# Kernel optimization log

Measured on AMD Instinct MI355X. Metric: run time of the kernel, lower is better.

## Reference

```python
import jax, jax.numpy as jnp
import numpy as np

B, T = 64, 2048
RNN_DIM, EMB_DIM, ATTN_DIM = 1024, 512, 128
N_FILT, KSIZE = 32, 31
PAD = (KSIZE - 1) // 2


def setup_inputs() -> dict:
    key = jax.random.key(0)
    ks = jax.random.split(key, 8)
    s = 0.02
    return {
        "attention_hidden_state": jax.random.normal(ks[0], (B, RNN_DIM), jnp.float32),
        "memory": jax.random.normal(ks[1], (B, T, EMB_DIM), jnp.float32),
        "processed_memory": jax.random.normal(ks[2], (B, T, ATTN_DIM), jnp.float32),
        "attention_weights_cat": jax.random.uniform(ks[3], (B, 2, T), jnp.float32),
        "mask": jnp.zeros((B, T), dtype=bool),
        "Wq": jax.random.normal(ks[4], (ATTN_DIM, RNN_DIM), jnp.float32) * s,
        "Wconv": jax.random.normal(ks[5], (N_FILT, 2, KSIZE), jnp.float32) * s,
        "Wloc": jax.random.normal(ks[6], (ATTN_DIM, N_FILT), jnp.float32) * s,
        "Wv": jax.random.normal(ks[7], (1, ATTN_DIM), jnp.float32) * s,
    }


def reference(attention_hidden_state, memory, processed_memory,
              attention_weights_cat, mask, Wq, Wconv, Wloc, Wv):
    # query projection: [B, rnn] -> [B, 1, attn]
    pq = jnp.einsum("br,ar->ba", attention_hidden_state, Wq)[:, None, :]
    # location conv: [B, 2, T] -> [B, F, T]
    conv = jax.lax.conv_general_dilated(
        attention_weights_cat, Wconv, window_strides=(1,),
        padding=[(PAD, PAD)], dimension_numbers=("NCH", "OIH", "NCH"))
    # [B, T, F] @ Wloc.T -> [B, T, attn]
    ploc = jnp.einsum("bft,af->bta", conv, Wloc)
    # energies: [B, T]
    energies = jnp.einsum("bta,oa->bto", jnp.tanh(pq + ploc + processed_memory), Wv)[..., 0]
    alignment = jnp.where(mask, -jnp.inf, energies)
    attention_weights = jax.nn.softmax(alignment, axis=1)
    # context: [B, emb]
    attention_context = jnp.einsum("bt,bte->be", attention_weights, memory)
    return attention_context, attention_weights
```

## Files before the change

### kernel.cpp

```cpp
#include <hip/hip_runtime.h>
#include <math.h>

#define BB 64
#define TT 2048
#define RNN 1024
#define EMB 512
#define ATTN 128
#define NF 32
#define KS 31
#define PADW 15

#define CHUNK 64
#define NCH (TT / CHUNK)

__device__ __forceinline__ float fast_tanh(float x) {
    float ax = fabsf(x);
    float e = __expf(-2.f * ax);
    float r = (1.f - e) * __builtin_amdgcn_rcpf(1.f + e);
    return copysignf(r, x);
}

__global__ __launch_bounds__(256) void pq_kernel(const float* __restrict__ h,
                                                 const float* __restrict__ Wq,
                                                 float* __restrict__ pq) {
    int b = blockIdx.x >> 2;
    int q = blockIdx.x & 3;
    __shared__ float s_h[RNN];
    for (int i = threadIdx.x; i < RNN; i += 256) s_h[i] = h[b * RNN + i];
    __syncthreads();

    int wave = threadIdx.x >> 6;
    int lane = threadIdx.x & 63;
#pragma unroll 2
    for (int j = 0; j < 8; ++j) {
        int a = q * 32 + wave * 8 + j;
        const float4* wq4 = (const float4*)(Wq + (size_t)a * RNN);
        float acc = 0.f;
#pragma unroll
        for (int i = 0; i < 4; ++i) {
            float4 w4 = wq4[lane + 64 * i];
            float4 h4 = *(const float4*)(s_h + 4 * (lane + 64 * i));
            acc += w4.x * h4.x + w4.y * h4.y + w4.z * h4.z + w4.w * h4.w;
        }
#pragma unroll
        for (int off = 32; off > 0; off >>= 1) acc += __shfl_xor(acc, off, 64);
        if (lane == 0) pq[b * ATTN + a] = acc;
    }
}

__global__ __launch_bounds__(256) void fused_kernel(
    const float* __restrict__ pm,
    const float* __restrict__ awc,
    const float* __restrict__ mem,
    const unsigned char* __restrict__ mask,
    const float* __restrict__ pq,
    const float* __restrict__ Wconv,
    const float* __restrict__ Wloc,
    const float* __restrict__ Wv,
    float* __restrict__ wp,
    float* __restrict__ ms,
    float* __restrict__ cp)
{
    int b = blockIdx.x >> 5;
    int ch = blockIdx.x & 31;
    int t0 = ch * CHUNK;
    int tid = threadIdx.x;

    __shared__ float s_awc[2][CHUNK + 2 * PADW];
    __shared__ float s_conv[CHUNK][36];
    __shared__ float s_e[CHUNK];
    __shared__ float s_p[CHUNK];

    for (int i = tid; i < 2 * (CHUNK + 2 * PADW); i += 256) {
        int c = i / (CHUNK + 2 * PADW);
        int j = i % (CHUNK + 2 * PADW);
        int tg = t0 - PADW + j;
        s_awc[c][j] = (tg >= 0 && tg < TT) ? awc[((size_t)b * 2 + c) * TT + tg] : 0.f;
    }
    __syncthreads();

    {
        int t = tid & 63;
        int fh = tid >> 6;
        float aw[2][KS];
#pragma unroll
        for (int c = 0; c < 2; ++c)
#pragma unroll
            for (int k = 0; k < KS; ++k) aw[c][k] = s_awc[c][t + k];
#pragma unroll
        for (int ff = 0; ff < 8; ++ff) {
            int f = fh * 8 + ff;
            float acc = 0.f;
#pragma unroll
            for (int c = 0; c < 2; ++c)
#pragma unroll
                for (int k = 0; k < KS; ++k)
                    acc += aw[c][k] * Wconv[(f * 2 + c) * KS + k];
            s_conv[t][f] = acc;
        }
    }
    __syncthreads();

    int wave = tid >> 6;
    int lane = tid & 63;

    float wl0[NF], wl1[NF];
#pragma unroll
    for (int f = 0; f < NF; ++f) {
        wl0[f] = Wloc[lane * NF + f];
        wl1[f] = Wloc[(lane + 64) * NF + f];
    }
    float pq0 = pq[b * ATTN + lane], pq1 = pq[b * ATTN + lane + 64];
    float wv0 = Wv[lane], wv1 = Wv[lane + 64];

    float eout = 0.f;
#pragma unroll 2
    for (int i = 0; i < 16; ++i) {
        int tl = wave * 16 + i;
        int tg = t0 + tl;
        float v0 = pq0, v1 = pq1;
        const float4* cv4 = (const float4*)&s_conv[tl][0];
#pragma unroll
        for (int f4 = 0; f4 < 8; ++f4) {
            float4 cv = cv4[f4];
            v0 += cv.x * wl0[f4 * 4 + 0] + cv.y * wl0[f4 * 4 + 1] +
                  cv.z * wl0[f4 * 4 + 2] + cv.w * wl0[f4 * 4 + 3];
            v1 += cv.x * wl1[f4 * 4 + 0] + cv.y * wl1[f4 * 4 + 1] +
                  cv.z * wl1[f4 * 4 + 2] + cv.w * wl1[f4 * 4 + 3];
        }
        const float* pmrow = pm + ((size_t)(b * TT + tg)) * ATTN;
        v0 += pmrow[lane];
        v1 += pmrow[lane + 64];
        float e = wv0 * fast_tanh(v0) + wv1 * fast_tanh(v1);
#pragma unroll
        for (int off = 32; off > 0; off >>= 1) e += __shfl_xor(e, off, 64);
        if (lane == i) eout = e;
    }
    if (lane < 16) {
        int tl = wave * 16 + lane;
        float e = eout;
        if (mask[(size_t)b * TT + t0 + tl] != 0) e = -1e30f;
        s_e[tl] = e;
    }
    __syncthreads();

    float m = s_e[lane];
#pragma unroll
    for (int off = 32; off > 0; off >>= 1) m = fmaxf(m, __shfl_xor(m, off, 64));

    if (tid < CHUNK) {
        float p = __expf(s_e[tid] - m);
        s_p[tid] = p;
        wp[(size_t)b * TT + t0 + tid] = p;
    }
    __syncthreads();

    float ssum = s_p[lane];
#pragma unroll
    for (int off = 32; off > 0; off >>= 1) ssum += __shfl_xor(ssum, off, 64);
    if (tid == 0) {
        ms[(b * NCH + ch) * 2 + 0] = m;
        ms[(b * NCH + ch) * 2 + 1] = ssum;
    }

    int e4 = tid & 127;
    int half = tid >> 7;
    float4 acc = {0.f, 0.f, 0.f, 0.f};
    const float4* m4 = (const float4*)(mem + ((size_t)b * TT + t0) * EMB) +
                       (size_t)half * (EMB / 4) + e4;
#pragma unroll 8
    for (int i = 0; i < CHUNK / 2; ++i) {
        float pv = s_p[2 * i + half];
        float4 mv = m4[(size_t)i * (2 * EMB / 4)];
        acc.x += pv * mv.x;
        acc.y += pv * mv.y;
        acc.z += pv * mv.z;
        acc.w += pv * mv.w;
    }
    float4* cp4 = (float4*)(cp + ((size_t)((ch * 2 + half) * BB + b)) * EMB) + e4;
    *cp4 = acc;
}

__global__ __launch_bounds__(256) void combine_kernel(
    const float* __restrict__ wp, const float* __restrict__ ms,
    const float* __restrict__ cp, float* __restrict__ ctx,
    float* __restrict__ wts) {
    int b = blockIdx.x;
    int tid = threadIdx.x;
    __shared__ float s_m[NCH], s_s[NCH], s_scale[NCH];
    if (tid < NCH) {
        s_m[tid] = ms[(b * NCH + tid) * 2 + 0];
        s_s[tid] = ms[(b * NCH + tid) * 2 + 1];
    }
    __syncthreads();
    float M = -1e30f;
#pragma unroll
    for (int c = 0; c < NCH; ++c) M = fmaxf(M, s_m[c]);
    float S = 0.f;
#pragma unroll
    for (int c = 0; c < NCH; ++c) S += s_s[c] * __expf(s_m[c] - M);
    float invS = 1.f / S;
    if (tid < NCH) s_scale[tid] = __expf(s_m[tid] - M) * invS;
    __syncthreads();

    if (tid < 128) {
        float4 acc = {0.f, 0.f, 0.f, 0.f};
#pragma unroll 8
        for (int c = 0; c < 2 * NCH; ++c) {
            float sc = s_scale[c >> 1];
            float4 v = *((const float4*)(cp + ((size_t)(c * BB + b)) * EMB) + tid);
            acc.x += sc * v.x;
            acc.y += sc * v.y;
            acc.z += sc * v.z;
            acc.w += sc * v.w;
        }
        *((float4*)(ctx + (size_t)b * EMB) + tid) = acc;
    }
#pragma unroll
    for (int i = 0; i < 8; ++i) {
        int t = i * 256 + tid;
        wts[(size_t)b * TT + t] = wp[(size_t)b * TT + t] * s_scale[t >> 6];
    }
}

extern "C" void kernel_launch(void* const* d_in, const int* in_sizes, int n_in,
                              void* d_out, int out_size, void* d_ws, size_t ws_size,
                              hipStream_t stream) {
    const float* h    = (const float*)d_in[0];
    const float* mem  = (const float*)d_in[1];
    const float* pmem = (const float*)d_in[2];
    const float* awc  = (const float*)d_in[3];
    const unsigned char* mask = (const unsigned char*)d_in[4];
    const float* Wq   = (const float*)d_in[5];
    const float* Wcv  = (const float*)d_in[6];
    const float* Wloc = (const float*)d_in[7];
    const float* Wv   = (const float*)d_in[8];

    float* out = (float*)d_out;
    float* ctx = out;
    float* wts = out + BB * EMB;

    float* ws = (float*)d_ws;
    float* pq = ws;
    float* wp = pq + BB * ATTN;
    float* ms = wp + BB * TT;
    float* cp = ms + BB * NCH * 2;

    pq_kernel<<<BB * 4, 256, 0, stream>>>(h, Wq, pq);
    fused_kernel<<<BB * NCH, 256, 0, stream>>>(pmem, awc, mem, mask, pq, Wcv,
                                               Wloc, Wv, wp, ms, cp);
    combine_kernel<<<BB, 256, 0, stream>>>(wp, ms, cp, ctx, wts);
}
```

Before: 126.4 us.

## Make each wave own a 16-step softmax chunk to remove block barriers

Each wave now handles its own 16-timestep chunk end to end: it batches the processed_memory loads, keeps the 16 energies in registers, runs a batched shuffle reduction, computes the local max/sum, and accumulates its own memory context. Three block barriers and the shared-memory energy and probability staging go away, and memory loads per wave become independent. The cost is four times as many partial chunks (128 per batch), so the combine kernel reads more partial context data. The extra registers for the per-wave arrays may pressure the 4-blocks-per-CU launch bound.

```diff
diff --git a/kernel.cpp b/kernel.cpp
--- a/kernel.cpp
+++ b/kernel.cpp
@@ -10,8 +10,9 @@
 #define KS 31
 #define PADW 15
 
-#define CHUNK 64
-#define NCH (TT / CHUNK)
+#define CHW 16
+#define NCH (TT / CHW)
+#define BLK_T 64
 
 __device__ __forceinline__ float fast_tanh(float x) {
     float ax = fabsf(x);
@@ -48,7 +49,7 @@
     }
 }
 
-__global__ __launch_bounds__(256) void fused_kernel(
+__global__ __launch_bounds__(256, 4) void fused_kernel(
     const float* __restrict__ pm,
     const float* __restrict__ awc,
     const float* __restrict__ mem,
@@ -62,26 +63,27 @@
     float* __restrict__ cp)
 {
     int b = blockIdx.x >> 5;
-    int ch = blockIdx.x & 31;
-    int t0 = ch * CHUNK;
+    int chg = blockIdx.x & 31;
+    int t0b = chg * BLK_T;
     int tid = threadIdx.x;
-
-    __shared__ float s_awc[2][CHUNK + 2 * PADW];
-    __shared__ float s_conv[CHUNK][36];
-    __shared__ float s_e[CHUNK];
-    __shared__ float s_p[CHUNK];
-
-    for (int i = tid; i < 2 * (CHUNK + 2 * PADW); i += 256) {
-        int c = i / (CHUNK + 2 * PADW);
-        int j = i % (CHUNK + 2 * PADW);
-        int tg = t0 - PADW + j;
+    int w = tid >> 6;
+    int lane = tid & 63;
+    int ch = chg * 4 + w;
+    int t0w = ch * CHW;
+
+    __shared__ float s_awc[2][BLK_T + 2 * PADW + 2];
+    __shared__ float s_conv[BLK_T][36];
+
+    for (int i = tid; i < 2 * (BLK_T + 2 * PADW); i += 256) {
+        int c = i / (BLK_T + 2 * PADW);
+        int j = i % (BLK_T + 2 * PADW);
+        int tg = t0b - PADW + j;
         s_awc[c][j] = (tg >= 0 && tg < TT) ? awc[((size_t)b * 2 + c) * TT + tg] : 0.f;
     }
     __syncthreads();
 
     {
         int t = tid & 63;
-        int fh = tid >> 6;
         float aw[2][KS];
 #pragma unroll
         for (int c = 0; c < 2; ++c)
@@ -89,7 +91,7 @@
             for (int k = 0; k < KS; ++k) aw[c][k] = s_awc[c][t + k];
 #pragma unroll
         for (int ff = 0; ff < 8; ++ff) {
-            int f = fh * 8 + ff;
+            int f = w * 8 + ff;
             float acc = 0.f;
 #pragma unroll
             for (int c = 0; c < 2; ++c)
@@ -101,9 +103,6 @@
     }
     __syncthreads();
 
-    int wave = tid >> 6;
-    int lane = tid & 63;
-
     float wl0[NF], wl1[NF];
 #pragma unroll
     for (int f = 0; f < NF; ++f) {
@@ -113,72 +112,83 @@
     float pq0 = pq[b * ATTN + lane], pq1 = pq[b * ATTN + lane + 64];
     float wv0 = Wv[lane], wv1 = Wv[lane + 64];
 
-    float eout = 0.f;
-#pragma unroll 2
-    for (int i = 0; i < 16; ++i) {
-        int tl = wave * 16 + i;
-        int tg = t0 + tl;
-        float v0 = pq0, v1 = pq1;
-        const float4* cv4 = (const float4*)&s_conv[tl][0];
-#pragma unroll
-        for (int f4 = 0; f4 < 8; ++f4) {
-            float4 cv = cv4[f4];
-            v0 += cv.x * wl0[f4 * 4 + 0] + cv.y * wl0[f4 * 4 + 1] +
-                  cv.z * wl0[f4 * 4 + 2] + cv.w * wl0[f4 * 4 + 3];
-            v1 += cv.x * wl1[f4 * 4 + 0] + cv.y * wl1[f4 * 4 + 1] +
-                  cv.z * wl1[f4 * 4 + 2] + cv.w * wl1[f4 * 4 + 3];
-        }
-        const float* pmrow = pm + ((size_t)(b * TT + tg)) * ATTN;
-        v0 += pmrow[lane];
-        v1 += pmrow[lane + 64];
-        float e = wv0 * fast_tanh(v0) + wv1 * fast_tanh(v1);
-#pragma unroll
-        for (int off = 32; off > 0; off >>= 1) e += __shfl_xor(e, off, 64);
-        if (lane == i) eout = e;
-    }
-    if (lane < 16) {
-        int tl = wave * 16 + lane;
-        float e = eout;
-        if (mask[(size_t)b * TT + t0 + tl] != 0) e = -1e30f;
-        s_e[tl] = e;
-    }
-    __syncthreads();
-
-    float m = s_e[lane];
-#pragma unroll
-    for (int off = 32; off > 0; off >>= 1) m = fmaxf(m, __shfl_xor(m, off, 64));
-
-    if (tid < CHUNK) {
-        float p = __expf(s_e[tid] - m);
-        s_p[tid] = p;
-        wp[(size_t)b * TT + t0 + tid] = p;
-    }
-    __syncthreads();
-
-    float ssum = s_p[lane];
-#pragma unroll
-    for (int off = 32; off > 0; off >>= 1) ssum += __shfl_xor(ssum, off, 64);
-    if (tid == 0) {
-        ms[(b * NCH + ch) * 2 + 0] = m;
-        ms[(b * NCH + ch) * 2 + 1] = ssum;
-    }
-
-    int e4 = tid & 127;
-    int half = tid >> 7;
-    float4 acc = {0.f, 0.f, 0.f, 0.f};
-    const float4* m4 = (const float4*)(mem + ((size_t)b * TT + t0) * EMB) +
-                       (size_t)half * (EMB / 4) + e4;
-#pragma unroll 8
-    for (int i = 0; i < CHUNK / 2; ++i) {
-        float pv = s_p[2 * i + half];
-        float4 mv = m4[(size_t)i * (2 * EMB / 4)];
-        acc.x += pv * mv.x;
-        acc.y += pv * mv.y;
-        acc.z += pv * mv.z;
-        acc.w += pv * mv.w;
-    }
-    float4* cp4 = (float4*)(cp + ((size_t)((ch * 2 + half) * BB + b)) * EMB) + e4;
-    *cp4 = acc;
+    float e[CHW];
+#pragma unroll
+    for (int h = 0; h < 2; ++h) {
+        float pA[8], pB[8];
+#pragma unroll
+        for (int i = 0; i < 8; ++i) {
+            const float* r = pm + ((size_t)b * TT + t0w + h * 8 + i) * ATTN;
+            pA[i] = r[lane];
+            pB[i] = r[lane + 64];
+        }
+#pragma unroll
+        for (int i = 0; i < 8; ++i) {
+            int tl = w * CHW + h * 8 + i;
+            float v0 = pq0 + pA[i], v1 = pq1 + pB[i];
+            const float4* cv4 = (const float4*)&s_conv[tl][0];
+#pragma unroll
+            for (int f4 = 0; f4 < 8; ++f4) {
+                float4 cv = cv4[f4];
+                v0 += cv.x * wl0[f4 * 4 + 0] + cv.y * wl0[f4 * 4 + 1] +
+                      cv.z * wl0[f4 * 4 + 2] + cv.w * wl0[f4 * 4 + 3];
+                v1 += cv.x * wl1[f4 * 4 + 0] + cv.y * wl1[f4 * 4 + 1] +
+                      cv.z * wl1[f4 * 4 + 2] + cv.w * wl1[f4 * 4 + 3];
+            }
+            e[h * 8 + i] = wv0 * fast_tanh(v0) + wv1 * fast_tanh(v1);
+        }
+    }
+
+#pragma unroll
+    for (int off = 32; off > 0; off >>= 1)
+#pragma unroll
+        for (int i = 0; i < CHW; ++i) e[i] += __shfl_xor(e[i], off, 64);
+
+    {
+        const unsigned int* mk4 = (const unsigned int*)(mask + (size_t)b * TT + t0w);
+#pragma unroll
+        for (int q = 0; q < 4; ++q) {
+            unsigned int mword = mk4[q];
+#pragma unroll
+            for (int j = 0; j < 4; ++j)
+                if ((mword >> (8 * j)) & 0xff) e[q * 4 + j] = -1e30f;
+        }
+    }
+
+    float m = e[0];
+#pragma unroll
+    for (int i = 1; i < CHW; ++i) m = fmaxf(m, e[i]);
+    float p[CHW], s = 0.f;
+#pragma unroll
+    for (int i = 0; i < CHW; ++i) {
+        p[i] = __expf(e[i] - m);
+        s += p[i];
+    }
+    if (lane == 0) {
+        ms[((size_t)b * NCH + ch) * 2 + 0] = m;
+        ms[((size_t)b * NCH + ch) * 2 + 1] = s;
+    }
+    {
+        float pv = p[0];
+#pragma unroll
+        for (int i = 1; i < CHW; ++i)
+            if (lane == i) pv = p[i];
+        if (lane < CHW) wp[(size_t)b * TT + t0w + lane] = pv;
+    }
+
+    float4 a0 = {0.f, 0.f, 0.f, 0.f}, a1 = {0.f, 0.f, 0.f, 0.f};
+    const float4* m4 = (const float4*)(mem + ((size_t)b * TT + t0w) * EMB);
+#pragma unroll
+    for (int i = 0; i < CHW; ++i) {
+        float pi = p[i];
+        float4 v0 = m4[(size_t)i * (EMB / 4) + lane];
+        float4 v1 = m4[(size_t)i * (EMB / 4) + 64 + lane];
+        a0.x += pi * v0.x; a0.y += pi * v0.y; a0.z += pi * v0.z; a0.w += pi * v0.w;
+        a1.x += pi * v1.x; a1.y += pi * v1.y; a1.z += pi * v1.z; a1.w += pi * v1.w;
+    }
+    float4* cp4 = (float4*)(cp + ((size_t)b * NCH + ch) * EMB);
+    cp4[lane] = a0;
+    cp4[64 + lane] = a1;
 }
 
 __global__ __launch_bounds__(256) void combine_kernel(
@@ -189,37 +199,36 @@
     int tid = threadIdx.x;
     __shared__ float s_m[NCH], s_s[NCH], s_scale[NCH];
     if (tid < NCH) {
-        s_m[tid] = ms[(b * NCH + tid) * 2 + 0];
-        s_s[tid] = ms[(b * NCH + tid) * 2 + 1];
+        s_m[tid] = ms[((size_t)b * NCH + tid) * 2 + 0];
+        s_s[tid] = ms[((size_t)b * NCH + tid) * 2 + 1];
     }
     __syncthreads();
     float M = -1e30f;
-#pragma unroll
+#pragma unroll 8
     for (int c = 0; c < NCH; ++c) M = fmaxf(M, s_m[c]);
     float S = 0.f;
-#pragma unroll
+#pragma unroll 8
     for (int c = 0; c < NCH; ++c) S += s_s[c] * __expf(s_m[c] - M);
     float invS = 1.f / S;
     if (tid < NCH) s_scale[tid] = __expf(s_m[tid] - M) * invS;
     __syncthreads();
 
-    if (tid < 128) {
-        float4 acc = {0.f, 0.f, 0.f, 0.f};
-#pragma unroll 8
-        for (int c = 0; c < 2 * NCH; ++c) {
-            float sc = s_scale[c >> 1];
-            float4 v = *((const float4*)(cp + ((size_t)(c * BB + b)) * EMB) + tid);
+    {
+        float2 acc = {0.f, 0.f};
+        const float2* cp2 = (const float2*)(cp + (size_t)b * NCH * EMB);
+#pragma unroll 4
+        for (int c = 0; c < NCH; ++c) {
+            float sc = s_scale[c];
+            float2 v = cp2[(size_t)c * (EMB / 2) + tid];
             acc.x += sc * v.x;
             acc.y += sc * v.y;
-            acc.z += sc * v.z;
-            acc.w += sc * v.w;
-        }
-        *((float4*)(ctx + (size_t)b * EMB) + tid) = acc;
+        }
+        ((float2*)(ctx + (size_t)b * EMB))[tid] = acc;
     }
 #pragma unroll
     for (int i = 0; i < 8; ++i) {
         int t = i * 256 + tid;
-        wts[(size_t)b * TT + t] = wp[(size_t)b * TT + t] * s_scale[t >> 6];
+        wts[(size_t)b * TT + t] = wp[(size_t)b * TT + t] * s_scale[t >> 4];
     }
 }
 
@@ -247,7 +256,7 @@
     float* cp = ms + BB * NCH * 2;
 
     pq_kernel<<<BB * 4, 256, 0, stream>>>(h, Wq, pq);
-    fused_kernel<<<BB * NCH, 256, 0, stream>>>(pmem, awc, mem, mask, pq, Wcv,
-                                               Wloc, Wv, wp, ms, cp);
+    fused_kernel<<<BB * 32, 256, 0, stream>>>(pmem, awc, mem, mask, pq, Wcv,
+                                              Wloc, Wv, wp, ms, cp);
     combine_kernel<<<BB, 256, 0, stream>>>(wp, ms, cp, ctx, wts);
 }
```

Result: slower. 322.0 us (+154.7%).

## Split fused energy/context kernel into separate energy, scale, context, reduce passes

Applied to the files above, without the earlier changes.

The energy computation and the memory-weighted context accumulation are split out of the single fused kernel. Context is now computed in a separate pass that uses the already-normalized weights, and a reduction kernel sums the partial results. This shortens the fused kernel, which may help occupancy and scheduling. In exchange it adds two extra launches and a serialization point before the large memory read, so that read can no longer overlap with the energy work.

```diff
diff --git a/kernel.cpp b/kernel.cpp
--- a/kernel.cpp
+++ b/kernel.cpp
@@ -13,6 +13,10 @@
 #define CHUNK 64
 #define NCH (TT / CHUNK)
 
+#define SEG_T 64
+#define NSEG (TT / SEG_T)
+#define NPART (NSEG * 2)
+
 __device__ __forceinline__ float fast_tanh(float x) {
     float ax = fabsf(x);
     float e = __expf(-2.f * ax);
@@ -48,18 +52,16 @@
     }
 }
 
-__global__ __launch_bounds__(256) void fused_kernel(
+__global__ __launch_bounds__(256) void energy_kernel(
     const float* __restrict__ pm,
     const float* __restrict__ awc,
-    const float* __restrict__ mem,
     const unsigned char* __restrict__ mask,
     const float* __restrict__ pq,
     const float* __restrict__ Wconv,
     const float* __restrict__ Wloc,
     const float* __restrict__ Wv,
     float* __restrict__ wp,
-    float* __restrict__ ms,
-    float* __restrict__ cp)
+    float* __restrict__ ms)
 {
     int b = blockIdx.x >> 5;
     int ch = blockIdx.x & 31;
@@ -159,68 +161,76 @@
 #pragma unroll
     for (int off = 32; off > 0; off >>= 1) ssum += __shfl_xor(ssum, off, 64);
     if (tid == 0) {
-        ms[(b * NCH + ch) * 2 + 0] = m;
-        ms[(b * NCH + ch) * 2 + 1] = ssum;
-    }
-
-    int e4 = tid & 127;
-    int half = tid >> 7;
-    float4 acc = {0.f, 0.f, 0.f, 0.f};
-    const float4* m4 = (const float4*)(mem + ((size_t)b * TT + t0) * EMB) +
-                       (size_t)half * (EMB / 4) + e4;
-#pragma unroll 8
-    for (int i = 0; i < CHUNK / 2; ++i) {
-        float pv = s_p[2 * i + half];
-        float4 mv = m4[(size_t)i * (2 * EMB / 4)];
-        acc.x += pv * mv.x;
-        acc.y += pv * mv.y;
-        acc.z += pv * mv.z;
-        acc.w += pv * mv.w;
-    }
-    float4* cp4 = (float4*)(cp + ((size_t)((ch * 2 + half) * BB + b)) * EMB) + e4;
-    *cp4 = acc;
-}
-
-__global__ __launch_bounds__(256) void combine_kernel(
+        ms[((size_t)b * NCH + ch) * 2 + 0] = m;
+        ms[((size_t)b * NCH + ch) * 2 + 1] = ssum;
+    }
+}
+
+__global__ __launch_bounds__(256) void scales_kernel(
     const float* __restrict__ wp, const float* __restrict__ ms,
-    const float* __restrict__ cp, float* __restrict__ ctx,
     float* __restrict__ wts) {
     int b = blockIdx.x;
     int tid = threadIdx.x;
     __shared__ float s_m[NCH], s_s[NCH], s_scale[NCH];
     if (tid < NCH) {
-        s_m[tid] = ms[(b * NCH + tid) * 2 + 0];
-        s_s[tid] = ms[(b * NCH + tid) * 2 + 1];
+        s_m[tid] = ms[((size_t)b * NCH + tid) * 2 + 0];
+        s_s[tid] = ms[((size_t)b * NCH + tid) * 2 + 1];
     }
     __syncthreads();
     float M = -1e30f;
-#pragma unroll
+#pragma unroll 8
     for (int c = 0; c < NCH; ++c) M = fmaxf(M, s_m[c]);
     float S = 0.f;
-#pragma unroll
+#pragma unroll 8
     for (int c = 0; c < NCH; ++c) S += s_s[c] * __expf(s_m[c] - M);
     float invS = 1.f / S;
     if (tid < NCH) s_scale[tid] = __expf(s_m[tid] - M) * invS;
     __syncthreads();
-
-    if (tid < 128) {
-        float4 acc = {0.f, 0.f, 0.f, 0.f};
-#pragma unroll 8
-        for (int c = 0; c < 2 * NCH; ++c) {
-            float sc = s_scale[c >> 1];
-            float4 v = *((const float4*)(cp + ((size_t)(c * BB + b)) * EMB) + tid);
-            acc.x += sc * v.x;
-            acc.y += sc * v.y;
-            acc.z += sc * v.z;
-            acc.w += sc * v.w;
-        }
-        *((float4*)(ctx + (size_t)b * EMB) + tid) = acc;
-    }
 #pragma unroll
     for (int i = 0; i < 8; ++i) {
         int t = i * 256 + tid;
         wts[(size_t)b * TT + t] = wp[(size_t)b * TT + t] * s_scale[t >> 6];
     }
+}
+
+__global__ __launch_bounds__(256) void ctx_partial_kernel(
+    const float* __restrict__ mem,
+    const float* __restrict__ wts,
+    float* __restrict__ partial)
+{
+    int b = blockIdx.x >> 5;
+    int seg = blockIdx.x & 31;
+    int tid = threadIdx.x;
+    int e4 = tid & 127;
+    int half = tid >> 7;
+
+    __shared__ float s_w[SEG_T];
+    if (tid < SEG_T) s_w[tid] = wts[(size_t)b * TT + seg * SEG_T + tid];
+    __syncthreads();
+
+    float4 acc = {0.f, 0.f, 0.f, 0.f};
+    const float4* m4 = (const float4*)(mem + ((size_t)b * TT + seg * SEG_T) * EMB) +
+                       (size_t)half * (EMB / 4) + e4;
+#pragma unroll 8
+    for (int i = 0; i < SEG_T / 2; ++i) {
+        float wv = s_w[2 * i + half];
+        float4 mv = m4[(size_t)i * (2 * EMB / 4)];
+        acc.x += wv * mv.x;
+        acc.y += wv * mv.y;
+        acc.z += wv * mv.z;
+        acc.w += wv * mv.w;
+    }
+    float4* p4 = (float4*)(partial + ((size_t)(seg * 2 + half) * BB + b) * EMB) + e4;
+    *p4 = acc;
+}
+
+__global__ __launch_bounds__(256) void ctx_reduce_kernel(
+    const float* __restrict__ partial, float* __restrict__ ctx) {
+    int idx = blockIdx.x * 256 + threadIdx.x;
+    float acc = 0.f;
+#pragma unroll 8
+    for (int s = 0; s < NPART; ++s) acc += partial[(size_t)s * (BB * EMB) + idx];
+    ctx[idx] = acc;
 }
 
 extern "C" void kernel_launch(void* const* d_in, const int* in_sizes, int n_in,
@@ -244,10 +254,12 @@
     float* pq = ws;
     float* wp = pq + BB * ATTN;
     float* ms = wp + BB * TT;
-    float* cp = ms + BB * NCH * 2;
+    float* partial = ms + BB * NCH * 2;
 
     pq_kernel<<<BB * 4, 256, 0, stream>>>(h, Wq, pq);
-    fused_kernel<<<BB * NCH, 256, 0, stream>>>(pmem, awc, mem, mask, pq, Wcv,
-                                               Wloc, Wv, wp, ms, cp);
-    combine_kernel<<<BB, 256, 0, stream>>>(wp, ms, cp, ctx, wts);
-}
+    energy_kernel<<<BB * NCH, 256, 0, stream>>>(pmem, awc, mask, pq, Wcv, Wloc,
+                                                Wv, wp, ms);
+    scales_kernel<<<BB, 256, 0, stream>>>(wp, ms, wts);
+    ctx_partial_kernel<<<BB * NSEG, 256, 0, stream>>>(mem, wts, partial);
+    ctx_reduce_kernel<<<(BB * EMB) / 256, 256, 0, stream>>>(partial, ctx);
+}
```

Result: slower. 147.4 us (+16.6%).
